# Kernel tuning notes

Hardware: AMD Instinct MI355X
Metric: run time of the kernel (lower is better)

The kernel has to match this reference:

```python
import jax, jax.numpy as jnp
import numpy as np

B, S, H, L, D, DI = 4, 32, 8, 128, 512, 2048
EPS = 1e-6
TEMP = float(D) ** 0.5


def layer_norm(x, g, b):
    mu = jnp.mean(x, axis=-1, keepdims=True)
    var = jnp.mean((x - mu) ** 2, axis=-1, keepdims=True)
    return (x - mu) * jax.lax.rsqrt(var + EPS) * g + b


def setup_inputs() -> dict:
    key = jax.random.key(0)
    ks = jax.random.split(key, 8)
    x = jax.random.normal(ks[0], (B, S, L, D), jnp.float32)
    mask = jax.random.randint(ks[1], (B, S, L), 0, 2, jnp.int32)
    # learned params
    w = jax.random.normal(ks[2], (1, 1, H, L, D), jnp.float32) * (1.0 / np.sqrt(D))
    v_w = jax.random.normal(ks[3], (D, D), jnp.float32) * 0.02   # nn.Linear weight (out,in)
    ln_g = jnp.ones((D,), jnp.float32)
    ln_b = jnp.zeros((D,), jnp.float32)
    w1 = jax.random.normal(ks[4], (DI, D), jnp.float32) * 0.02
    b1 = jnp.zeros((DI,), jnp.float32)
    w2 = jax.random.normal(ks[5], (D, DI), jnp.float32) * 0.02
    b2 = jnp.zeros((D,), jnp.float32)
    fln_g = jnp.ones((D,), jnp.float32)
    fln_b = jnp.zeros((D,), jnp.float32)
    return {"x": x, "mask": mask, "w": w, "v_w": v_w, "ln_g": ln_g, "ln_b": ln_b,
            "w1": w1, "b1": b1, "w2": w2, "b2": b2, "fln_g": fln_g, "fln_b": fln_b}


def reference(x, mask, w, v_w, ln_g, ln_b, w1, b1, w2, b2, fln_g, fln_b):
    # attn logits: broadcast mul + reduce over d_model == einsum over d
    attn = jnp.einsum('bsld,hld->bshl', x, w[0, 0]) / TEMP           # (B,S,H,L)
    attn = jnp.where(mask[:, :, None, :] == 0, -1e9, attn)
    attn = jax.nn.softmax(attn, axis=-1)                              # dropout: eval mode
    v = jnp.einsum('bsld,ed->bsle', x, v_w)                           # Linear no bias: x @ W.T
    out = jnp.einsum('bsld,bshl->bshd', v, attn)                      # weighted sum readout
    out = layer_norm(out, ln_g, ln_b)
    # PositionwiseFeedForward with residual + LayerNorm
    h = jax.nn.relu(jnp.einsum('bshd,fd->bshf', out, w1) + b1)
    y = jnp.einsum('bshf,df->bshd', h, w2) + b2 + out
    y = layer_norm(y, fln_g, fln_b)
    return y, attn
```

## Files before the change

### kernel.cpp

```cpp
#include <hip/hip_runtime.h>
#include <hip/hip_bf16.h>

#define BB 4
#define SS 32
#define HH 8
#define LL 128
#define DD 512
#define DI 2048
#define EPSN 1e-6f
#define INV_TEMP 0.04419417382415922f

#define NLOGIT_BLK 4096
#define NCAST_GRAN ((DI*DD/4)*2 + (DD*DD/4))
#define NCAST_BLK (NCAST_GRAN / 256)

#define NROW (BB*SS*HH)
#define SLICE ((size_t)NROW * DD)

typedef __attribute__((ext_vector_type(8))) short short8;
typedef __attribute__((ext_vector_type(4))) float float4v;

static __device__ __forceinline__ unsigned short f2b(float f) {
  __hip_bfloat16 h = __float2bfloat16(f);
  return *(unsigned short*)&h;
}

__global__ __launch_bounds__(256) void pre_kernel(
    const float* __restrict__ x, const int* __restrict__ mask,
    const float* __restrict__ w, const float* __restrict__ w1,
    const float* __restrict__ w2, const float* __restrict__ v_w,
    unsigned short* __restrict__ w1b, unsigned short* __restrict__ w2b,
    unsigned short* __restrict__ v_wb, float* __restrict__ logits) {
  int blk = blockIdx.x;
  if (blk < NLOGIT_BLK) {
    int wv = threadIdx.x >> 6, lane = threadIdx.x & 63;
    int p  = blk * 4 + wv;
    int bs = p >> 7, l = p & (LL - 1);

    const float4* xr = (const float4*)(x + ((size_t)bs * LL + l) * DD) + lane * 2;
    float4 x0 = xr[0], x1 = xr[1];

    float acc[HH];
#pragma unroll
    for (int h = 0; h < HH; ++h) {
      const float4* wr = (const float4*)(w + ((size_t)h * LL + l) * DD) + lane * 2;
      float4 w0 = wr[0], w1v = wr[1];
      acc[h] = x0.x * w0.x + x0.y * w0.y + x0.z * w0.z + x0.w * w0.w +
               x1.x * w1v.x + x1.y * w1v.y + x1.z * w1v.z + x1.w * w1v.w;
    }
#pragma unroll
    for (int off = 32; off > 0; off >>= 1) {
#pragma unroll
      for (int h = 0; h < HH; ++h) acc[h] += __shfl_xor(acc[h], off);
    }
    if (lane == 0) {
      int msk = mask[bs * LL + l];
#pragma unroll
      for (int h = 0; h < HH; ++h) {
        float lg = msk ? acc[h] * INV_TEMP : -1e9f;
        logits[((size_t)bs * HH + h) * LL + l] = lg;
      }
    }
  } else {
    const int n1 = (DI * DD) / 4;
    const int n2 = n1;
    int i = (blk - NLOGIT_BLK) * 256 + threadIdx.x;
    const float4* src;
    unsigned short* dst;
    int j = i;
    if (i < n1)           { src = (const float4*)w1;  dst = w1b; }
    else if (i < n1 + n2) { src = (const float4*)w2;  dst = w2b;  j = i - n1; }
    else                  { src = (const float4*)v_w; dst = v_wb; j = i - n1 - n2; }
    float4 v = src[j];
    dst[j * 4 + 0] = f2b(v.x);
    dst[j * 4 + 1] = f2b(v.y);
    dst[j * 4 + 2] = f2b(v.z);
    dst[j * 4 + 3] = f2b(v.w);
  }
}

__global__ __launch_bounds__(512) void xa_kernel(
    const float* __restrict__ x, const float* __restrict__ logits,
    float* __restrict__ attn_out, unsigned short* __restrict__ xab) {
  int bs = blockIdx.x >> 1, half = blockIdx.x & 1;
  int t = threadIdx.x, wv = t >> 6, lane = t & 63;

  __shared__ float sattn_t[LL][HH];
  __shared__ float sxa[2][HH][256];

  if (wv < 4) {
    for (int h = wv; h < HH; h += 4) {
      const float* lg = logits + ((size_t)bs * HH + h) * LL;
      float v0 = lg[lane], v1 = lg[lane + 64];
      float m = fmaxf(v0, v1);
#pragma unroll
      for (int off = 32; off > 0; off >>= 1) m = fmaxf(m, __shfl_xor(m, off));
      float e0 = __expf(v0 - m), e1 = __expf(v1 - m);
      float s = e0 + e1;
#pragma unroll
      for (int off = 32; off > 0; off >>= 1) s += __shfl_xor(s, off);
      float inv = 1.f / s;
      e0 *= inv; e1 *= inv;
      sattn_t[lane][h]      = e0;
      sattn_t[lane + 64][h] = e1;
      if (half == 0) {
        float* ao = attn_out + ((size_t)bs * HH + h) * LL;
        ao[lane]      = e0;
        ao[lane + 64] = e1;
      }
    }
  }
  __syncthreads();

  int col = t & 255, lseg = t >> 8;
  int e = half * 256 + col;
  const float* xb = x + (size_t)bs * LL * DD;
  float acc[HH];
#pragma unroll
  for (int h = 0; h < HH; ++h) acc[h] = 0.f;
  int l0 = lseg * 64;
  for (int l = l0; l < l0 + 64; ++l) {
    float xv = xb[(size_t)l * DD + e];
    float4 a0 = *(const float4*)&sattn_t[l][0];
    float4 a1 = *(const float4*)&sattn_t[l][4];
    acc[0] += a0.x * xv; acc[1] += a0.y * xv;
    acc[2] += a0.z * xv; acc[3] += a0.w * xv;
    acc[4] += a1.x * xv; acc[5] += a1.y * xv;
    acc[6] += a1.z * xv; acc[7] += a1.w * xv;
  }
#pragma unroll
  for (int h = 0; h < HH; ++h) sxa[lseg][h][col] = acc[h];
  __syncthreads();
  if (t < 256) {
    unsigned short* xo = xab + (size_t)bs * HH * DD;
#pragma unroll
    for (int h = 0; h < HH; ++h)
      xo[h * DD + t + half * 256] = f2b(sxa[0][h][t] + sxa[1][h][t]);
  }
}

__global__ __launch_bounds__(256) void gemm_v_kernel(
    const unsigned short* __restrict__ xab, const unsigned short* __restrict__ v_wb,
    float* __restrict__ vpart) {
  int blk = blockIdx.x;
  int nt = blk & 7, mt = (blk >> 3) & 15, kslice = blk >> 7;
  int wv = threadIdx.x >> 6, lane = threadIdx.x & 63;
  int lm = lane & 15, lq = lane >> 4;

  int m0 = mt * 64 + wv * 16;
  int n0 = nt * 64;
  int g0 = kslice * 16;

  const short8* A0 = (const short8*)(xab + (size_t)(m0 + lm) * DD) + g0;
  const short8* Bp[4];
#pragma unroll
  for (int nf = 0; nf < 4; ++nf)
    Bp[nf] = (const short8*)(v_wb + (size_t)(n0 + nf * 16 + lm) * DD) + g0;

  float4v acc[4];
#pragma unroll
  for (int nf = 0; nf < 4; ++nf) acc[nf] = (float4v){0.f, 0.f, 0.f, 0.f};

#pragma unroll
  for (int ks = 0; ks < 4; ++ks) {
    short8 a0 = A0[ks * 4 + lq];
    short8 b[4];
#pragma unroll
    for (int nf = 0; nf < 4; ++nf) b[nf] = Bp[nf][ks * 4 + lq];
#pragma unroll
    for (int nf = 0; nf < 4; ++nf)
      acc[nf] = __builtin_amdgcn_mfma_f32_16x16x32_bf16(a0, b[nf], acc[nf], 0, 0, 0);
  }

  float* outp = vpart + (size_t)kslice * SLICE;
#pragma unroll
  for (int nf = 0; nf < 4; ++nf) {
    int col = n0 + nf * 16 + lm;
#pragma unroll
    for (int r = 0; r < 4; ++r) {
      int row = m0 + lq * 4 + r;
      outp[(size_t)row * DD + col] = acc[nf][r];
    }
  }
}

__global__ __launch_bounds__(256) void ln_mid_kernel(
    const float* __restrict__ vpart, const float* __restrict__ ln_g,
    const float* __restrict__ ln_b, float* __restrict__ o_ln,
    unsigned short* __restrict__ o_lnb) {
  int wv = threadIdx.x >> 6, lane = threadIdx.x & 63;
  int row = blockIdx.x * 4 + wv;

  const float* p0 = vpart + (size_t)row * DD;
  float vals[8];
  float sum = 0.f, sq = 0.f;
#pragma unroll
  for (int k = 0; k < 8; ++k) {
    int d = lane + 64 * k;
    float v = p0[d] + p0[SLICE + d] + p0[2 * SLICE + d] + p0[3 * SLICE + d];
    vals[k] = v;
    sum += v;
    sq += v * v;
  }
#pragma unroll
  for (int off = 32; off > 0; off >>= 1) {
    sum += __shfl_xor(sum, off);
    sq  += __shfl_xor(sq, off);
  }
  float mu  = sum * (1.f / DD);
  float var = sq * (1.f / DD) - mu * mu;
  float rs  = rsqrtf(var + EPSN);
  float* op = o_ln + (size_t)row * DD;
  unsigned short* opb = o_lnb + (size_t)row * DD;
#pragma unroll
  for (int k = 0; k < 8; ++k) {
    int d = lane + 64 * k;
    float v = (vals[k] - mu) * rs * ln_g[d] + ln_b[d];
    op[d]  = v;
    opb[d] = f2b(v);
  }
}

__global__ __launch_bounds__(256) void gemm1_kernel(
    const unsigned short* __restrict__ xb, const unsigned short* __restrict__ w1b,
    const float* __restrict__ b1, unsigned short* __restrict__ h1b) {
  int blk = blockIdx.x;
  int nt = blk & 31, mt = blk >> 5;
  int wv = threadIdx.x >> 6, lane = threadIdx.x & 63;
  int lm = lane & 15, lq = lane >> 4;

  int m0 = mt * 64 + wv * 16;
  int n0 = nt * 64;

  const short8* A0 = (const short8*)(xb + (size_t)(m0 + lm) * DD);
  const short8* Bp[4];
#pragma unroll
  for (int nf = 0; nf < 4; ++nf)
    Bp[nf] = (const short8*)(w1b + (size_t)(n0 + nf * 16 + lm) * DD);

  float4v acc[4];
#pragma unroll
  for (int nf = 0; nf < 4; ++nf) acc[nf] = (float4v){0.f, 0.f, 0.f, 0.f};

#pragma unroll 4
  for (int ks = 0; ks < DD / 32; ++ks) {
    short8 a0 = A0[ks * 4 + lq];
    short8 b[4];
#pragma unroll
    for (int nf = 0; nf < 4; ++nf) b[nf] = Bp[nf][ks * 4 + lq];
#pragma unroll
    for (int nf = 0; nf < 4; ++nf)
      acc[nf] = __builtin_amdgcn_mfma_f32_16x16x32_bf16(a0, b[nf], acc[nf], 0, 0, 0);
  }

#pragma unroll
  for (int nf = 0; nf < 4; ++nf) {
    int col = n0 + nf * 16 + lm;
    float bb = b1[col];
#pragma unroll
    for (int r = 0; r < 4; ++r) {
      int row = m0 + lq * 4 + r;
      float v = acc[nf][r] + bb;
      h1b[(size_t)row * DI + col] = f2b(fmaxf(v, 0.f));
    }
  }
}

__global__ __launch_bounds__(256) void gemm2_kernel(
    const unsigned short* __restrict__ h1b, const unsigned short* __restrict__ w2b,
    float* __restrict__ ypart) {
  int blk = blockIdx.x;
  int nt = blk & 7, mt = (blk >> 3) & 15, kslice = blk >> 7;
  int wv = threadIdx.x >> 6, lane = threadIdx.x & 63;
  int lm = lane & 15, lq = lane >> 4;

  int m0 = mt * 64 + wv * 16;
  int n0 = nt * 64;
  int g0 = kslice * 64;

  const short8* A0 = (const short8*)(h1b + (size_t)(m0 + lm) * DI) + g0;
  const short8* Bp[4];
#pragma unroll
  for (int nf = 0; nf < 4; ++nf)
    Bp[nf] = (const short8*)(w2b + (size_t)(n0 + nf * 16 + lm) * DI) + g0;

  float4v acc[4];
#pragma unroll
  for (int nf = 0; nf < 4; ++nf) acc[nf] = (float4v){0.f, 0.f, 0.f, 0.f};

#pragma unroll 4
  for (int ks = 0; ks < 16; ++ks) {
    short8 a0 = A0[ks * 4 + lq];
    short8 b[4];
#pragma unroll
    for (int nf = 0; nf < 4; ++nf) b[nf] = Bp[nf][ks * 4 + lq];
#pragma unroll
    for (int nf = 0; nf < 4; ++nf)
      acc[nf] = __builtin_amdgcn_mfma_f32_16x16x32_bf16(a0, b[nf], acc[nf], 0, 0, 0);
  }

  float* outp = ypart + (size_t)kslice * SLICE;
#pragma unroll
  for (int nf = 0; nf < 4; ++nf) {
    int col = n0 + nf * 16 + lm;
#pragma unroll
    for (int r = 0; r < 4; ++r) {
      int row = m0 + lq * 4 + r;
      outp[(size_t)row * DD + col] = acc[nf][r];
    }
  }
}

__global__ __launch_bounds__(256) void ln_final_kernel(
    const float* __restrict__ ypart, const float* __restrict__ o_ln,
    const float* __restrict__ b2, const float* __restrict__ fln_g,
    const float* __restrict__ fln_b, float* __restrict__ y_out) {
  int wv = threadIdx.x >> 6, lane = threadIdx.x & 63;
  int row = blockIdx.x * 4 + wv;

  const float* p0 = ypart + (size_t)row * DD;
  const float* ol = o_ln + (size_t)row * DD;
  float vals[8];
  float sum = 0.f, sq = 0.f;
#pragma unroll
  for (int k = 0; k < 8; ++k) {
    int d = lane + 64 * k;
    float v = p0[d] + p0[SLICE + d] + p0[2 * SLICE + d] + p0[3 * SLICE + d] +
              b2[d] + ol[d];
    vals[k] = v;
    sum += v;
    sq += v * v;
  }
#pragma unroll
  for (int off = 32; off > 0; off >>= 1) {
    sum += __shfl_xor(sum, off);
    sq  += __shfl_xor(sq, off);
  }
  float mu  = sum * (1.f / DD);
  float var = sq * (1.f / DD) - mu * mu;
  float rs  = rsqrtf(var + EPSN);
  float* yo = y_out + (size_t)row * DD;
#pragma unroll
  for (int k = 0; k < 8; ++k) {
    int d = lane + 64 * k;
    yo[d] = (vals[k] - mu) * rs * fln_g[d] + fln_b[d];
  }
}

extern "C" void kernel_launch(void* const* d_in, const int* in_sizes, int n_in,
                              void* d_out, int out_size, void* d_ws, size_t ws_size,
                              hipStream_t stream) {
  const float* x     = (const float*)d_in[0];
  const int*   mask  = (const int*)d_in[1];
  const float* w     = (const float*)d_in[2];
  const float* v_w   = (const float*)d_in[3];
  const float* ln_g  = (const float*)d_in[4];
  const float* ln_b  = (const float*)d_in[5];
  const float* w1    = (const float*)d_in[6];
  const float* b1    = (const float*)d_in[7];
  const float* w2    = (const float*)d_in[8];
  const float* b2    = (const float*)d_in[9];
  const float* fln_g = (const float*)d_in[10];
  const float* fln_b = (const float*)d_in[11];

  float* y    = (float*)d_out;
  float* attn = y + (size_t)BB * SS * HH * DD;

  char* ws = (char*)d_ws;
  float*          o_ln    = (float*)(ws);
  unsigned short* o_lnb   = (unsigned short*)(ws + 2097152);
  unsigned short* w1b     = (unsigned short*)(ws + 3145728);
  unsigned short* w2b     = (unsigned short*)(ws + 5242880);
  unsigned short* h1b     = (unsigned short*)(ws + 7340032);
  float*          ypart   = (float*)(ws + 11534336);
  unsigned short* v_wb    = (unsigned short*)(ws + 19922944);
  unsigned short* xab     = (unsigned short*)(ws + 20447232);
  float*          vpart   = (float*)(ws + 21495808);
  float*          logits  = (float*)(ws + 29884416);

  pre_kernel<<<NLOGIT_BLK + NCAST_BLK, 256, 0, stream>>>(
      x, mask, w, w1, w2, v_w, w1b, w2b, v_wb, logits);
  xa_kernel<<<BB * SS * 2, 512, 0, stream>>>(x, logits, attn, xab);
  gemm_v_kernel<<<512, 256, 0, stream>>>(xab, v_wb, vpart);
  ln_mid_kernel<<<256, 256, 0, stream>>>(vpart, ln_g, ln_b, o_ln, o_lnb);
  gemm1_kernel<<<512, 256, 0, stream>>>(o_lnb, w1b, b1, h1b);
  gemm2_kernel<<<512, 256, 0, stream>>>(h1b, w2b, ypart);
  ln_final_kernel<<<256, 256, 0, stream>>>(ypart, o_ln, b2, fln_g, fln_b, y);
}
```

Before: 172.6 us.

## Fuse attention readout, V projection and mid LayerNorm into one kernel

Merges the softmax/attention-weighted x reduction, the bf16 MFMA V-projection GEMM and the first LayerNorm into a single kernel, one block per (b,s). The intermediate xa activations stay in shared memory as bf16 and the V output stays in shared memory in fp32, so the xab buffer, the split-K vpart partial sums and two kernel launches are no longer needed. The cost is less parallelism: 128 blocks instead of 256, each thread reducing over all 128 rows of x. Every block also re-reads the full V weight matrix through cache, and half of each MFMA A tile is padding rows whose results are thrown away.

```diff
diff --git a/kernel.cpp b/kernel.cpp
--- a/kernel.cpp
+++ b/kernel.cpp
@@ -16,6 +16,7 @@
 
 #define NROW (BB*SS*HH)
 #define SLICE ((size_t)NROW * DD)
+#define SXAP (DD + 8)
 
 typedef __attribute__((ext_vector_type(8))) short short8;
 typedef __attribute__((ext_vector_type(4))) float float4v;
@@ -79,14 +80,17 @@
   }
 }
 
-__global__ __launch_bounds__(512) void xa_kernel(
+__global__ __launch_bounds__(512) void xa_v_ln_kernel(
     const float* __restrict__ x, const float* __restrict__ logits,
-    float* __restrict__ attn_out, unsigned short* __restrict__ xab) {
-  int bs = blockIdx.x >> 1, half = blockIdx.x & 1;
+    const unsigned short* __restrict__ v_wb, const float* __restrict__ ln_g,
+    const float* __restrict__ ln_b, float* __restrict__ attn_out,
+    float* __restrict__ o_ln, unsigned short* __restrict__ o_lnb) {
+  int bs = blockIdx.x;
   int t = threadIdx.x, wv = t >> 6, lane = t & 63;
 
   __shared__ float sattn_t[LL][HH];
-  __shared__ float sxa[2][HH][256];
+  __shared__ unsigned short sxa[16][SXAP];
+  __shared__ float sout[HH][DD];
 
   if (wv < 4) {
     for (int h = wv; h < HH; h += 4) {
@@ -103,121 +107,96 @@
       e0 *= inv; e1 *= inv;
       sattn_t[lane][h]      = e0;
       sattn_t[lane + 64][h] = e1;
-      if (half == 0) {
-        float* ao = attn_out + ((size_t)bs * HH + h) * LL;
-        ao[lane]      = e0;
-        ao[lane + 64] = e1;
+      float* ao = attn_out + ((size_t)bs * HH + h) * LL;
+      ao[lane]      = e0;
+      ao[lane + 64] = e1;
+    }
+  }
+  __syncthreads();
+
+  {
+    int e = t;
+    const float* xb = x + (size_t)bs * LL * DD;
+    float acc[HH];
+#pragma unroll
+    for (int h = 0; h < HH; ++h) acc[h] = 0.f;
+    for (int l = 0; l < LL; ++l) {
+      float xv = xb[(size_t)l * DD + e];
+      float4 a0 = *(const float4*)&sattn_t[l][0];
+      float4 a1 = *(const float4*)&sattn_t[l][4];
+      acc[0] += a0.x * xv; acc[1] += a0.y * xv;
+      acc[2] += a0.z * xv; acc[3] += a0.w * xv;
+      acc[4] += a1.x * xv; acc[5] += a1.y * xv;
+      acc[6] += a1.z * xv; acc[7] += a1.w * xv;
+    }
+#pragma unroll
+    for (int h = 0; h < HH; ++h) sxa[h][e] = f2b(acc[h]);
+  }
+  __syncthreads();
+
+  {
+    int lm = lane & 15, lq = lane >> 4;
+    int n0 = wv * 64;
+    const short8* Bp[4];
+#pragma unroll
+    for (int nf = 0; nf < 4; ++nf)
+      Bp[nf] = (const short8*)(v_wb + (size_t)(n0 + nf * 16 + lm) * DD);
+
+    float4v acc[4];
+#pragma unroll
+    for (int nf = 0; nf < 4; ++nf) acc[nf] = (float4v){0.f, 0.f, 0.f, 0.f};
+
+#pragma unroll 4
+    for (int ks = 0; ks < DD / 32; ++ks) {
+      short8 a0 = *(const short8*)&sxa[lm][ks * 32 + lq * 8];
+      short8 b[4];
+#pragma unroll
+      for (int nf = 0; nf < 4; ++nf) b[nf] = Bp[nf][ks * 4 + lq];
+#pragma unroll
+      for (int nf = 0; nf < 4; ++nf)
+        acc[nf] = __builtin_amdgcn_mfma_f32_16x16x32_bf16(a0, b[nf], acc[nf], 0, 0, 0);
+    }
+
+#pragma unroll
+    for (int nf = 0; nf < 4; ++nf) {
+      int col = n0 + nf * 16 + lm;
+#pragma unroll
+      for (int r = 0; r < 4; ++r) {
+        int row = lq * 4 + r;
+        if (row < HH) sout[row][col] = acc[nf][r];
       }
     }
   }
   __syncthreads();
 
-  int col = t & 255, lseg = t >> 8;
-  int e = half * 256 + col;
-  const float* xb = x + (size_t)bs * LL * DD;
-  float acc[HH];
-#pragma unroll
-  for (int h = 0; h < HH; ++h) acc[h] = 0.f;
-  int l0 = lseg * 64;
-  for (int l = l0; l < l0 + 64; ++l) {
-    float xv = xb[(size_t)l * DD + e];
-    float4 a0 = *(const float4*)&sattn_t[l][0];
-    float4 a1 = *(const float4*)&sattn_t[l][4];
-    acc[0] += a0.x * xv; acc[1] += a0.y * xv;
-    acc[2] += a0.z * xv; acc[3] += a0.w * xv;
-    acc[4] += a1.x * xv; acc[5] += a1.y * xv;
-    acc[6] += a1.z * xv; acc[7] += a1.w * xv;
-  }
-#pragma unroll
-  for (int h = 0; h < HH; ++h) sxa[lseg][h][col] = acc[h];
-  __syncthreads();
-  if (t < 256) {
-    unsigned short* xo = xab + (size_t)bs * HH * DD;
-#pragma unroll
-    for (int h = 0; h < HH; ++h)
-      xo[h * DD + t + half * 256] = f2b(sxa[0][h][t] + sxa[1][h][t]);
-  }
-}
-
-__global__ __launch_bounds__(256) void gemm_v_kernel(
-    const unsigned short* __restrict__ xab, const unsigned short* __restrict__ v_wb,
-    float* __restrict__ vpart) {
-  int blk = blockIdx.x;
-  int nt = blk & 7, mt = (blk >> 3) & 15, kslice = blk >> 7;
-  int wv = threadIdx.x >> 6, lane = threadIdx.x & 63;
-  int lm = lane & 15, lq = lane >> 4;
-
-  int m0 = mt * 64 + wv * 16;
-  int n0 = nt * 64;
-  int g0 = kslice * 16;
-
-  const short8* A0 = (const short8*)(xab + (size_t)(m0 + lm) * DD) + g0;
-  const short8* Bp[4];
-#pragma unroll
-  for (int nf = 0; nf < 4; ++nf)
-    Bp[nf] = (const short8*)(v_wb + (size_t)(n0 + nf * 16 + lm) * DD) + g0;
-
-  float4v acc[4];
-#pragma unroll
-  for (int nf = 0; nf < 4; ++nf) acc[nf] = (float4v){0.f, 0.f, 0.f, 0.f};
-
-#pragma unroll
-  for (int ks = 0; ks < 4; ++ks) {
-    short8 a0 = A0[ks * 4 + lq];
-    short8 b[4];
-#pragma unroll
-    for (int nf = 0; nf < 4; ++nf) b[nf] = Bp[nf][ks * 4 + lq];
-#pragma unroll
-    for (int nf = 0; nf < 4; ++nf)
-      acc[nf] = __builtin_amdgcn_mfma_f32_16x16x32_bf16(a0, b[nf], acc[nf], 0, 0, 0);
-  }
-
-  float* outp = vpart + (size_t)kslice * SLICE;
-#pragma unroll
-  for (int nf = 0; nf < 4; ++nf) {
-    int col = n0 + nf * 16 + lm;
-#pragma unroll
-    for (int r = 0; r < 4; ++r) {
-      int row = m0 + lq * 4 + r;
-      outp[(size_t)row * DD + col] = acc[nf][r];
-    }
-  }
-}
-
-__global__ __launch_bounds__(256) void ln_mid_kernel(
-    const float* __restrict__ vpart, const float* __restrict__ ln_g,
-    const float* __restrict__ ln_b, float* __restrict__ o_ln,
-    unsigned short* __restrict__ o_lnb) {
-  int wv = threadIdx.x >> 6, lane = threadIdx.x & 63;
-  int row = blockIdx.x * 4 + wv;
-
-  const float* p0 = vpart + (size_t)row * DD;
-  float vals[8];
-  float sum = 0.f, sq = 0.f;
-#pragma unroll
-  for (int k = 0; k < 8; ++k) {
-    int d = lane + 64 * k;
-    float v = p0[d] + p0[SLICE + d] + p0[2 * SLICE + d] + p0[3 * SLICE + d];
-    vals[k] = v;
-    sum += v;
-    sq += v * v;
-  }
-#pragma unroll
-  for (int off = 32; off > 0; off >>= 1) {
-    sum += __shfl_xor(sum, off);
-    sq  += __shfl_xor(sq, off);
-  }
-  float mu  = sum * (1.f / DD);
-  float var = sq * (1.f / DD) - mu * mu;
-  float rs  = rsqrtf(var + EPSN);
-  float* op = o_ln + (size_t)row * DD;
-  unsigned short* opb = o_lnb + (size_t)row * DD;
-#pragma unroll
-  for (int k = 0; k < 8; ++k) {
-    int d = lane + 64 * k;
-    float v = (vals[k] - mu) * rs * ln_g[d] + ln_b[d];
-    op[d]  = v;
-    opb[d] = f2b(v);
+  {
+    int r = wv;
+    float vals[8];
+    float sum = 0.f, sq = 0.f;
+#pragma unroll
+    for (int k = 0; k < 8; ++k) {
+      float v = sout[r][lane + 64 * k];
+      vals[k] = v;
+      sum += v;
+      sq += v * v;
+    }
+#pragma unroll
+    for (int off = 32; off > 0; off >>= 1) {
+      sum += __shfl_xor(sum, off);
+      sq  += __shfl_xor(sq, off);
+    }
+    float mu  = sum * (1.f / DD);
+    float var = sq * (1.f / DD) - mu * mu;
+    float rs  = rsqrtf(var + EPSN);
+    float* op = o_ln + ((size_t)bs * HH + r) * DD;
+    unsigned short* opb = o_lnb + ((size_t)bs * HH + r) * DD;
+#pragma unroll
+    for (int k = 0; k < 8; ++k) {
+      int d = lane + 64 * k;
+      float v = (vals[k] - mu) * rs * ln_g[d] + ln_b[d];
+      op[d]  = v;
+      opb[d] = f2b(v);
+    }
   }
 }
 
@@ -374,15 +353,12 @@
   unsigned short* h1b     = (unsigned short*)(ws + 7340032);
   float*          ypart   = (float*)(ws + 11534336);
   unsigned short* v_wb    = (unsigned short*)(ws + 19922944);
-  unsigned short* xab     = (unsigned short*)(ws + 20447232);
-  float*          vpart   = (float*)(ws + 21495808);
-  float*          logits  = (float*)(ws + 29884416);
+  float*          logits  = (float*)(ws + 20447232);
 
   pre_kernel<<<NLOGIT_BLK + NCAST_BLK, 256, 0, stream>>>(
       x, mask, w, w1, w2, v_w, w1b, w2b, v_wb, logits);
-  xa_kernel<<<BB * SS * 2, 512, 0, stream>>>(x, logits, attn, xab);
-  gemm_v_kernel<<<512, 256, 0, stream>>>(xab, v_wb, vpart);
-  ln_mid_kernel<<<256, 256, 0, stream>>>(vpart, ln_g, ln_b, o_ln, o_lnb);
+  xa_v_ln_kernel<<<BB * SS, 512, 0, stream>>>(
+      x, logits, v_wb, ln_g, ln_b, attn, o_ln, o_lnb);
   gemm1_kernel<<<512, 256, 0, stream>>>(o_lnb, w1b, b1, h1b);
   gemm2_kernel<<<512, 256, 0, stream>>>(h1b, w2b, ypart);
   ln_final_kernel<<<256, 256, 0, stream>>>(ypart, o_ln, b2, fln_g, fln_b, y);
```

After: 181.0 us. 4.8% more time.

## Fuse seven kernel launches into one cooperative persistent megakernel with grid syncs

Applied to the files above, without the earlier changes.

Replaces the seven-kernel launch chain with a single cooperative kernel of 256 blocks by 512 threads. The stages (weight cast plus logits, softmax plus attention readout, V GEMM, mid LayerNorm, FFN GEMM1, GEMM2, final LayerNorm) are separated by grid.sync. The aim is to remove per-launch overhead and the gaps between kernels. In exchange each stage runs on a fixed 256-block grid with less parallelism and a different work split, for example 4x fewer waves for the logits stage. The LayerNorm stages leave most blocks idle, and grid syncs carry their own cost. The old multi-kernel path is kept as a fallback if cooperative launch is unavailable.

```diff
diff --git a/kernel.cpp b/kernel.cpp
--- a/kernel.cpp
+++ b/kernel.cpp
@@ -1,5 +1,8 @@
 #include <hip/hip_runtime.h>
 #include <hip/hip_bf16.h>
+#include <hip/hip_cooperative_groups.h>
+
+namespace cg = cooperative_groups;
 
 #define BB 4
 #define SS 32
@@ -10,12 +13,15 @@
 #define EPSN 1e-6f
 #define INV_TEMP 0.04419417382415922f
 
-#define NLOGIT_BLK 4096
 #define NCAST_GRAN ((DI*DD/4)*2 + (DD*DD/4))
-#define NCAST_BLK (NCAST_GRAN / 256)
-
 #define NROW (BB*SS*HH)
 #define SLICE ((size_t)NROW * DD)
+
+#define GRID 256
+#define BLK  512
+
+#define NLOGIT_BLK 4096
+#define NCAST_BLK (NCAST_GRAN / 256)
 
 typedef __attribute__((ext_vector_type(8))) short short8;
 typedef __attribute__((ext_vector_type(4))) float float4v;
@@ -23,6 +29,305 @@
 static __device__ __forceinline__ unsigned short f2b(float f) {
   __hip_bfloat16 h = __float2bfloat16(f);
   return *(unsigned short*)&h;
+}
+
+struct MegaParams {
+  const float* x; const int* mask; const float* w; const float* v_w;
+  const float* ln_g; const float* ln_b;
+  const float* w1; const float* b1; const float* w2; const float* b2;
+  const float* fln_g; const float* fln_b;
+  float* y; float* attn;
+  unsigned short* w1b; unsigned short* w2b; unsigned short* v_wb;
+  unsigned short* o_lnb; unsigned short* h1b; unsigned short* xab;
+  float* logits; float* o_ln; float* vpart; float* ypart;
+};
+
+__global__ __launch_bounds__(BLK, 2) void mega_kernel(MegaParams p) {
+  cg::grid_group grid = cg::this_grid();
+  int blk = blockIdx.x;
+  int t = threadIdx.x, wv = t >> 6, lane = t & 63;
+  int lm = lane & 15, lq = lane >> 4;
+
+  __shared__ float sattn_t[LL][HH];
+  __shared__ float sxa[2][HH][256];
+
+  {
+    const int n1 = (DI * DD) / 4;
+    const int n2 = n1;
+    for (int i = blk * BLK + t; i < NCAST_GRAN; i += GRID * BLK) {
+      const float4* src;
+      unsigned short* dst;
+      int j = i;
+      if (i < n1)           { src = (const float4*)p.w1;  dst = p.w1b; }
+      else if (i < n1 + n2) { src = (const float4*)p.w2;  dst = p.w2b;  j = i - n1; }
+      else                  { src = (const float4*)p.v_w; dst = p.v_wb; j = i - n1 - n2; }
+      float4 v = src[j];
+      dst[j * 4 + 0] = f2b(v.x);
+      dst[j * 4 + 1] = f2b(v.y);
+      dst[j * 4 + 2] = f2b(v.z);
+      dst[j * 4 + 3] = f2b(v.w);
+    }
+  }
+  {
+    int gw = blk * 8 + wv;
+#pragma unroll
+    for (int i = 0; i < 8; ++i) {
+      int pp = gw * 8 + i;
+      int bs = pp >> 7, l = pp & (LL - 1);
+      const float4* xr = (const float4*)(p.x + ((size_t)bs * LL + l) * DD) + lane * 2;
+      float4 x0 = xr[0], x1 = xr[1];
+      float acc[HH];
+#pragma unroll
+      for (int h = 0; h < HH; ++h) {
+        const float4* wr = (const float4*)(p.w + ((size_t)h * LL + l) * DD) + lane * 2;
+        float4 w0 = wr[0], w1v = wr[1];
+        acc[h] = x0.x * w0.x + x0.y * w0.y + x0.z * w0.z + x0.w * w0.w +
+                 x1.x * w1v.x + x1.y * w1v.y + x1.z * w1v.z + x1.w * w1v.w;
+      }
+#pragma unroll
+      for (int off = 32; off > 0; off >>= 1) {
+#pragma unroll
+        for (int h = 0; h < HH; ++h) acc[h] += __shfl_xor(acc[h], off);
+      }
+      if (lane == 0) {
+        int msk = p.mask[bs * LL + l];
+#pragma unroll
+        for (int h = 0; h < HH; ++h) {
+          float lg = msk ? acc[h] * INV_TEMP : -1e9f;
+          p.logits[((size_t)bs * HH + h) * LL + l] = lg;
+        }
+      }
+    }
+  }
+  grid.sync();
+
+  {
+    int bs = blk >> 1, half = blk & 1;
+    if (wv < 4) {
+      for (int h = wv; h < HH; h += 4) {
+        const float* lg = p.logits + ((size_t)bs * HH + h) * LL;
+        float v0 = lg[lane], v1 = lg[lane + 64];
+        float m = fmaxf(v0, v1);
+#pragma unroll
+        for (int off = 32; off > 0; off >>= 1) m = fmaxf(m, __shfl_xor(m, off));
+        float e0 = __expf(v0 - m), e1 = __expf(v1 - m);
+        float s = e0 + e1;
+#pragma unroll
+        for (int off = 32; off > 0; off >>= 1) s += __shfl_xor(s, off);
+        float inv = 1.f / s;
+        e0 *= inv; e1 *= inv;
+        sattn_t[lane][h]      = e0;
+        sattn_t[lane + 64][h] = e1;
+        if (half == 0) {
+          float* ao = p.attn + ((size_t)bs * HH + h) * LL;
+          ao[lane]      = e0;
+          ao[lane + 64] = e1;
+        }
+      }
+    }
+    __syncthreads();
+
+    int col = t & 255, lseg = t >> 8;
+    int e = half * 256 + col;
+    const float* xb = p.x + (size_t)bs * LL * DD;
+    float acc[HH];
+#pragma unroll
+    for (int h = 0; h < HH; ++h) acc[h] = 0.f;
+    int l0 = lseg * 64;
+    for (int l = l0; l < l0 + 64; ++l) {
+      float xv = xb[(size_t)l * DD + e];
+      float4 a0 = *(const float4*)&sattn_t[l][0];
+      float4 a1 = *(const float4*)&sattn_t[l][4];
+      acc[0] += a0.x * xv; acc[1] += a0.y * xv;
+      acc[2] += a0.z * xv; acc[3] += a0.w * xv;
+      acc[4] += a1.x * xv; acc[5] += a1.y * xv;
+      acc[6] += a1.z * xv; acc[7] += a1.w * xv;
+    }
+#pragma unroll
+    for (int h = 0; h < HH; ++h) sxa[lseg][h][col] = acc[h];
+    __syncthreads();
+    if (t < 256) {
+      unsigned short* xo = p.xab + (size_t)bs * HH * DD;
+#pragma unroll
+      for (int h = 0; h < HH; ++h)
+        xo[h * DD + t + half * 256] = f2b(sxa[0][h][t] + sxa[1][h][t]);
+    }
+  }
+  grid.sync();
+
+  {
+    int ks = blk >> 7, rem = blk & 127;
+    int mt = rem >> 3, nt = rem & 7;
+    int m0 = mt * 64 + (wv & 3) * 16;
+    int n0 = nt * 64 + (wv >> 2) * 32;
+    int g0 = ks * 32;
+
+    const short8* A0 = (const short8*)(p.xab + (size_t)(m0 + lm) * DD) + g0;
+    const short8* Bp[2];
+#pragma unroll
+    for (int nf = 0; nf < 2; ++nf)
+      Bp[nf] = (const short8*)(p.v_wb + (size_t)(n0 + nf * 16 + lm) * DD) + g0;
+
+    float4v acc[2];
+#pragma unroll
+    for (int nf = 0; nf < 2; ++nf) acc[nf] = (float4v){0.f, 0.f, 0.f, 0.f};
+#pragma unroll 4
+    for (int ksi = 0; ksi < 8; ++ksi) {
+      short8 a0 = A0[ksi * 4 + lq];
+      short8 b[2];
+#pragma unroll
+      for (int nf = 0; nf < 2; ++nf) b[nf] = Bp[nf][ksi * 4 + lq];
+#pragma unroll
+      for (int nf = 0; nf < 2; ++nf)
+        acc[nf] = __builtin_amdgcn_mfma_f32_16x16x32_bf16(a0, b[nf], acc[nf], 0, 0, 0);
+    }
+    float* outp = p.vpart + (size_t)ks * SLICE;
+#pragma unroll
+    for (int nf = 0; nf < 2; ++nf) {
+      int col = n0 + nf * 16 + lm;
+#pragma unroll
+      for (int r = 0; r < 4; ++r)
+        outp[(size_t)(m0 + lq * 4 + r) * DD + col] = acc[nf][r];
+    }
+  }
+  grid.sync();
+
+  if (blk < 128) {
+    int row = blk * 8 + wv;
+    const float* p0 = p.vpart + (size_t)row * DD;
+    float vals[8];
+    float sum = 0.f, sq = 0.f;
+#pragma unroll
+    for (int k = 0; k < 8; ++k) {
+      int d = lane + 64 * k;
+      float v = p0[d] + p0[SLICE + d];
+      vals[k] = v;
+      sum += v;
+      sq += v * v;
+    }
+#pragma unroll
+    for (int off = 32; off > 0; off >>= 1) {
+      sum += __shfl_xor(sum, off);
+      sq  += __shfl_xor(sq, off);
+    }
+    float mu  = sum * (1.f / DD);
+    float var = sq * (1.f / DD) - mu * mu;
+    float rs  = rsqrtf(var + EPSN);
+    float* op = p.o_ln + (size_t)row * DD;
+    unsigned short* opb = p.o_lnb + (size_t)row * DD;
+#pragma unroll
+    for (int k = 0; k < 8; ++k) {
+      int d = lane + 64 * k;
+      float v = (vals[k] - mu) * rs * p.ln_g[d] + p.ln_b[d];
+      op[d]  = v;
+      opb[d] = f2b(v);
+    }
+  }
+  grid.sync();
+
+  {
+    int mt = blk >> 4, nt = blk & 15;
+    int m0 = mt * 64 + (wv & 3) * 16;
+    int n0 = nt * 128 + (wv >> 2) * 64;
+
+    const short8* A0 = (const short8*)(p.o_lnb + (size_t)(m0 + lm) * DD);
+    const short8* Bp[4];
+#pragma unroll
+    for (int nf = 0; nf < 4; ++nf)
+      Bp[nf] = (const short8*)(p.w1b + (size_t)(n0 + nf * 16 + lm) * DD);
+
+    float4v acc[4];
+#pragma unroll
+    for (int nf = 0; nf < 4; ++nf) acc[nf] = (float4v){0.f, 0.f, 0.f, 0.f};
+#pragma unroll 4
+    for (int ksi = 0; ksi < DD / 32; ++ksi) {
+      short8 a0 = A0[ksi * 4 + lq];
+      short8 b[4];
+#pragma unroll
+      for (int nf = 0; nf < 4; ++nf) b[nf] = Bp[nf][ksi * 4 + lq];
+#pragma unroll
+      for (int nf = 0; nf < 4; ++nf)
+        acc[nf] = __builtin_amdgcn_mfma_f32_16x16x32_bf16(a0, b[nf], acc[nf], 0, 0, 0);
+    }
+#pragma unroll
+    for (int nf = 0; nf < 4; ++nf) {
+      int col = n0 + nf * 16 + lm;
+      float bb = p.b1[col];
+#pragma unroll
+      for (int r = 0; r < 4; ++r) {
+        float v = acc[nf][r] + bb;
+        p.h1b[(size_t)(m0 + lq * 4 + r) * DI + col] = f2b(fmaxf(v, 0.f));
+      }
+    }
+  }
+  grid.sync();
+
+  {
+    int ks = blk >> 7, rem = blk & 127;
+    int mt = rem >> 3, nt = rem & 7;
+    int m0 = mt * 64 + (wv & 3) * 16;
+    int n0 = nt * 64 + (wv >> 2) * 32;
+    int g0 = ks * 128;
+
+    const short8* A0 = (const short8*)(p.h1b + (size_t)(m0 + lm) * DI) + g0;
+    const short8* Bp[2];
+#pragma unroll
+    for (int nf = 0; nf < 2; ++nf)
+      Bp[nf] = (const short8*)(p.w2b + (size_t)(n0 + nf * 16 + lm) * DI) + g0;
+
+    float4v acc[2];
+#pragma unroll
+    for (int nf = 0; nf < 2; ++nf) acc[nf] = (float4v){0.f, 0.f, 0.f, 0.f};
+#pragma unroll 4
+    for (int ksi = 0; ksi < 32; ++ksi) {
+      short8 a0 = A0[ksi * 4 + lq];
+      short8 b[2];
+#pragma unroll
+      for (int nf = 0; nf < 2; ++nf) b[nf] = Bp[nf][ksi * 4 + lq];
+#pragma unroll
+      for (int nf = 0; nf < 2; ++nf)
+        acc[nf] = __builtin_amdgcn_mfma_f32_16x16x32_bf16(a0, b[nf], acc[nf], 0, 0, 0);
+    }
+    float* outp = p.ypart + (size_t)ks * SLICE;
+#pragma unroll
+    for (int nf = 0; nf < 2; ++nf) {
+      int col = n0 + nf * 16 + lm;
+#pragma unroll
+      for (int r = 0; r < 4; ++r)
+        outp[(size_t)(m0 + lq * 4 + r) * DD + col] = acc[nf][r];
+    }
+  }
+  grid.sync();
+
+  if (blk < 128) {
+    int row = blk * 8 + wv;
+    const float* p0 = p.ypart + (size_t)row * DD;
+    const float* ol = p.o_ln + (size_t)row * DD;
+    float vals[8];
+    float sum = 0.f, sq = 0.f;
+#pragma unroll
+    for (int k = 0; k < 8; ++k) {
+      int d = lane + 64 * k;
+      float v = p0[d] + p0[SLICE + d] + p.b2[d] + ol[d];
+      vals[k] = v;
+      sum += v;
+      sq += v * v;
+    }
+#pragma unroll
+    for (int off = 32; off > 0; off >>= 1) {
+      sum += __shfl_xor(sum, off);
+      sq  += __shfl_xor(sq, off);
+    }
+    float mu  = sum * (1.f / DD);
+    float var = sq * (1.f / DD) - mu * mu;
+    float rs  = rsqrtf(var + EPSN);
+    float* yo = p.y + (size_t)row * DD;
+#pragma unroll
+    for (int k = 0; k < 8; ++k) {
+      int d = lane + 64 * k;
+      yo[d] = (vals[k] - mu) * rs * p.fln_g[d] + p.fln_b[d];
+    }
+  }
 }
 
 __global__ __launch_bounds__(256) void pre_kernel(
@@ -350,40 +655,54 @@
 extern "C" void kernel_launch(void* const* d_in, const int* in_sizes, int n_in,
                               void* d_out, int out_size, void* d_ws, size_t ws_size,
                               hipStream_t stream) {
-  const float* x     = (const float*)d_in[0];
-  const int*   mask  = (const int*)d_in[1];
-  const float* w     = (const float*)d_in[2];
-  const float* v_w   = (const float*)d_in[3];
-  const float* ln_g  = (const float*)d_in[4];
-  const float* ln_b  = (const float*)d_in[5];
-  const float* w1    = (const float*)d_in[6];
-  const float* b1    = (const float*)d_in[7];
-  const float* w2    = (const float*)d_in[8];
-  const float* b2    = (const float*)d_in[9];
-  const float* fln_g = (const float*)d_in[10];
-  const float* fln_b = (const float*)d_in[11];
-
-  float* y    = (float*)d_out;
-  float* attn = y + (size_t)BB * SS * HH * DD;
+  MegaParams hp;
+  hp.x     = (const float*)d_in[0];
+  hp.mask  = (const int*)d_in[1];
+  hp.w     = (const float*)d_in[2];
+  hp.v_w   = (const float*)d_in[3];
+  hp.ln_g  = (const float*)d_in[4];
+  hp.ln_b  = (const float*)d_in[5];
+  hp.w1    = (const float*)d_in[6];
+  hp.b1    = (const float*)d_in[7];
+  hp.w2    = (const float*)d_in[8];
+  hp.b2    = (const float*)d_in[9];
+  hp.fln_g = (const float*)d_in[10];
+  hp.fln_b = (const float*)d_in[11];
+
+  hp.y    = (float*)d_out;
+  hp.attn = hp.y + (size_t)BB * SS * HH * DD;
 
   char* ws = (char*)d_ws;
-  float*          o_ln    = (float*)(ws);
-  unsigned short* o_lnb   = (unsigned short*)(ws + 2097152);
-  unsigned short* w1b     = (unsigned short*)(ws + 3145728);
-  unsigned short* w2b     = (unsigned short*)(ws + 5242880);
-  unsigned short* h1b     = (unsigned short*)(ws + 7340032);
-  float*          ypart   = (float*)(ws + 11534336);
-  unsigned short* v_wb    = (unsigned short*)(ws + 19922944);
-  unsigned short* xab     = (unsigned short*)(ws + 20447232);
-  float*          vpart   = (float*)(ws + 21495808);
-  float*          logits  = (float*)(ws + 29884416);
-
-  pre_kernel<<<NLOGIT_BLK + NCAST_BLK, 256, 0, stream>>>(
-      x, mask, w, w1, w2, v_w, w1b, w2b, v_wb, logits);
-  xa_kernel<<<BB * SS * 2, 512, 0, stream>>>(x, logits, attn, xab);
-  gemm_v_kernel<<<512, 256, 0, stream>>>(xab, v_wb, vpart);
-  ln_mid_kernel<<<256, 256, 0, stream>>>(vpart, ln_g, ln_b, o_ln, o_lnb);
-  gemm1_kernel<<<512, 256, 0, stream>>>(o_lnb, w1b, b1, h1b);
-  gemm2_kernel<<<512, 256, 0, stream>>>(h1b, w2b, ypart);
-  ln_final_kernel<<<256, 256, 0, stream>>>(ypart, o_ln, b2, fln_g, fln_b, y);
-}
+  hp.o_ln   = (float*)(ws);
+  hp.o_lnb  = (unsigned short*)(ws + 2097152);
+  hp.w1b    = (unsigned short*)(ws + 3145728);
+  hp.w2b    = (unsigned short*)(ws + 5242880);
+  hp.h1b    = (unsigned short*)(ws + 7340032);
+  hp.ypart  = (float*)(ws + 11534336);
+  hp.v_wb   = (unsigned short*)(ws + 19922944);
+  hp.xab    = (unsigned short*)(ws + 20447232);
+  hp.vpart  = (float*)(ws + 21495808);
+  hp.logits = (float*)(ws + 29884416);
+
+  hipError_t err = hipErrorUnknown;
+  int coop = 0;
+  if (hipDeviceGetAttribute(&coop, hipDeviceAttributeCooperativeLaunch, 0) ==
+          hipSuccess && coop) {
+    void* args[] = { &hp };
+    err = hipLaunchCooperativeKernel((const void*)mega_kernel, dim3(GRID),
+                                     dim3(BLK), args, 0, stream);
+  }
+  if (err != hipSuccess) {
+    pre_kernel<<<NLOGIT_BLK + NCAST_BLK, 256, 0, stream>>>(
+        hp.x, hp.mask, hp.w, hp.w1, hp.w2, hp.v_w, hp.w1b, hp.w2b, hp.v_wb,
+        hp.logits);
+    xa_kernel<<<BB * SS * 2, 512, 0, stream>>>(hp.x, hp.logits, hp.attn, hp.xab);
+    gemm_v_kernel<<<512, 256, 0, stream>>>(hp.xab, hp.v_wb, hp.vpart);
+    ln_mid_kernel<<<256, 256, 0, stream>>>(hp.vpart, hp.ln_g, hp.ln_b, hp.o_ln,
+                                           hp.o_lnb);
+    gemm1_kernel<<<512, 256, 0, stream>>>(hp.o_lnb, hp.w1b, hp.b1, hp.h1b);
+    gemm2_kernel<<<512, 256, 0, stream>>>(hp.h1b, hp.w2b, hp.ypart);
+    ln_final_kernel<<<256, 256, 0, stream>>>(hp.ypart, hp.o_ln, hp.b2,
+                                             hp.fln_g, hp.fln_b, hp.y);
+  }
+}
```

Measured after the change: 377.9 us. 119% more time.

## Fuse value GEMM, both LayerNorms and FFN into one per-sequence kernel

Applied to the files above, without the earlier changes.

Replaces the five kernels after attention (value projection, mid LayerNorm, FFN GEMM1, FFN GEMM2, final LayerNorm) with a single kernel. Each block owns one (b,s) pair's eight rows and keeps every intermediate in shared memory: the normalized activations, the 2048-wide hidden layer and the partial outputs. This removes four launches, the split-K partial buffers and their global round trips. The cost is that only 128 blocks run, each re-reading all bf16 weights from cache. Half of each 16-row MFMA tile is idle because there are only eight rows, and the residual now uses the bf16-rounded LayerNorm output.

```diff
diff --git a/kernel.cpp b/kernel.cpp
--- a/kernel.cpp
+++ b/kernel.cpp
@@ -14,8 +14,9 @@
 #define NCAST_GRAN ((DI*DD/4)*2 + (DD*DD/4))
 #define NCAST_BLK (NCAST_GRAN / 256)
 
-#define NROW (BB*SS*HH)
-#define SLICE ((size_t)NROW * DD)
+#define SAS 520
+#define H1S 2056
+#define SYS 516
 
 typedef __attribute__((ext_vector_type(8))) short short8;
 typedef __attribute__((ext_vector_type(4))) float float4v;
@@ -23,6 +24,11 @@
 static __device__ __forceinline__ unsigned short f2b(float f) {
   __hip_bfloat16 h = __float2bfloat16(f);
   return *(unsigned short*)&h;
+}
+static __device__ __forceinline__ float b2f(unsigned short u) {
+  union { unsigned int i; float f; } v;
+  v.i = ((unsigned int)u) << 16;
+  return v.f;
 }
 
 __global__ __launch_bounds__(256) void pre_kernel(
@@ -139,211 +145,145 @@
   }
 }
 
-__global__ __launch_bounds__(256) void gemm_v_kernel(
+__global__ __launch_bounds__(512, 4) void megaffn_kernel(
     const unsigned short* __restrict__ xab, const unsigned short* __restrict__ v_wb,
-    float* __restrict__ vpart) {
-  int blk = blockIdx.x;
-  int nt = blk & 7, mt = (blk >> 3) & 15, kslice = blk >> 7;
-  int wv = threadIdx.x >> 6, lane = threadIdx.x & 63;
+    const float* __restrict__ ln_g, const float* __restrict__ ln_b,
+    const unsigned short* __restrict__ w1b, const float* __restrict__ b1,
+    const unsigned short* __restrict__ w2b, const float* __restrict__ b2,
+    const float* __restrict__ fln_g, const float* __restrict__ fln_b,
+    float* __restrict__ y_out) {
+  int bs = blockIdx.x;
+  int t = threadIdx.x, wv = t >> 6, lane = t & 63;
   int lm = lane & 15, lq = lane >> 4;
 
-  int m0 = mt * 64 + wv * 16;
-  int n0 = nt * 64;
-  int g0 = kslice * 16;
-
-  const short8* A0 = (const short8*)(xab + (size_t)(m0 + lm) * DD) + g0;
-  const short8* Bp[4];
-#pragma unroll
-  for (int nf = 0; nf < 4; ++nf)
-    Bp[nf] = (const short8*)(v_wb + (size_t)(n0 + nf * 16 + lm) * DD) + g0;
-
-  float4v acc[4];
-#pragma unroll
-  for (int nf = 0; nf < 4; ++nf) acc[nf] = (float4v){0.f, 0.f, 0.f, 0.f};
-
-#pragma unroll
-  for (int ks = 0; ks < 4; ++ks) {
-    short8 a0 = A0[ks * 4 + lq];
-    short8 b[4];
-#pragma unroll
-    for (int nf = 0; nf < 4; ++nf) b[nf] = Bp[nf][ks * 4 + lq];
-#pragma unroll
-    for (int nf = 0; nf < 4; ++nf)
-      acc[nf] = __builtin_amdgcn_mfma_f32_16x16x32_bf16(a0, b[nf], acc[nf], 0, 0, 0);
-  }
-
-  float* outp = vpart + (size_t)kslice * SLICE;
-#pragma unroll
-  for (int nf = 0; nf < 4; ++nf) {
-    int col = n0 + nf * 16 + lm;
-#pragma unroll
-    for (int r = 0; r < 4; ++r) {
-      int row = m0 + lq * 4 + r;
-      outp[(size_t)row * DD + col] = acc[nf][r];
-    }
-  }
-}
-
-__global__ __launch_bounds__(256) void ln_mid_kernel(
-    const float* __restrict__ vpart, const float* __restrict__ ln_g,
-    const float* __restrict__ ln_b, float* __restrict__ o_ln,
-    unsigned short* __restrict__ o_lnb) {
-  int wv = threadIdx.x >> 6, lane = threadIdx.x & 63;
-  int row = blockIdx.x * 4 + wv;
-
-  const float* p0 = vpart + (size_t)row * DD;
-  float vals[8];
-  float sum = 0.f, sq = 0.f;
-#pragma unroll
-  for (int k = 0; k < 8; ++k) {
-    int d = lane + 64 * k;
-    float v = p0[d] + p0[SLICE + d] + p0[2 * SLICE + d] + p0[3 * SLICE + d];
-    vals[k] = v;
-    sum += v;
-    sq += v * v;
-  }
-#pragma unroll
-  for (int off = 32; off > 0; off >>= 1) {
-    sum += __shfl_xor(sum, off);
-    sq  += __shfl_xor(sq, off);
-  }
-  float mu  = sum * (1.f / DD);
-  float var = sq * (1.f / DD) - mu * mu;
-  float rs  = rsqrtf(var + EPSN);
-  float* op = o_ln + (size_t)row * DD;
-  unsigned short* opb = o_lnb + (size_t)row * DD;
-#pragma unroll
-  for (int k = 0; k < 8; ++k) {
-    int d = lane + 64 * k;
-    float v = (vals[k] - mu) * rs * ln_g[d] + ln_b[d];
-    op[d]  = v;
-    opb[d] = f2b(v);
-  }
-}
-
-__global__ __launch_bounds__(256) void gemm1_kernel(
-    const unsigned short* __restrict__ xb, const unsigned short* __restrict__ w1b,
-    const float* __restrict__ b1, unsigned short* __restrict__ h1b) {
-  int blk = blockIdx.x;
-  int nt = blk & 31, mt = blk >> 5;
-  int wv = threadIdx.x >> 6, lane = threadIdx.x & 63;
-  int lm = lane & 15, lq = lane >> 4;
-
-  int m0 = mt * 64 + wv * 16;
-  int n0 = nt * 64;
-
-  const short8* A0 = (const short8*)(xb + (size_t)(m0 + lm) * DD);
-  const short8* Bp[4];
-#pragma unroll
-  for (int nf = 0; nf < 4; ++nf)
-    Bp[nf] = (const short8*)(w1b + (size_t)(n0 + nf * 16 + lm) * DD);
-
-  float4v acc[4];
-#pragma unroll
-  for (int nf = 0; nf < 4; ++nf) acc[nf] = (float4v){0.f, 0.f, 0.f, 0.f};
-
-#pragma unroll 4
-  for (int ks = 0; ks < DD / 32; ++ks) {
-    short8 a0 = A0[ks * 4 + lq];
-    short8 b[4];
-#pragma unroll
-    for (int nf = 0; nf < 4; ++nf) b[nf] = Bp[nf][ks * 4 + lq];
-#pragma unroll
-    for (int nf = 0; nf < 4; ++nf)
-      acc[nf] = __builtin_amdgcn_mfma_f32_16x16x32_bf16(a0, b[nf], acc[nf], 0, 0, 0);
-  }
-
-#pragma unroll
-  for (int nf = 0; nf < 4; ++nf) {
-    int col = n0 + nf * 16 + lm;
-    float bb = b1[col];
-#pragma unroll
-    for (int r = 0; r < 4; ++r) {
-      int row = m0 + lq * 4 + r;
-      float v = acc[nf][r] + bb;
-      h1b[(size_t)row * DI + col] = f2b(fmaxf(v, 0.f));
-    }
-  }
-}
-
-__global__ __launch_bounds__(256) void gemm2_kernel(
-    const unsigned short* __restrict__ h1b, const unsigned short* __restrict__ w2b,
-    float* __restrict__ ypart) {
-  int blk = blockIdx.x;
-  int nt = blk & 7, mt = (blk >> 3) & 15, kslice = blk >> 7;
-  int wv = threadIdx.x >> 6, lane = threadIdx.x & 63;
-  int lm = lane & 15, lq = lane >> 4;
-
-  int m0 = mt * 64 + wv * 16;
-  int n0 = nt * 64;
-  int g0 = kslice * 64;
-
-  const short8* A0 = (const short8*)(h1b + (size_t)(m0 + lm) * DI) + g0;
-  const short8* Bp[4];
-#pragma unroll
-  for (int nf = 0; nf < 4; ++nf)
-    Bp[nf] = (const short8*)(w2b + (size_t)(n0 + nf * 16 + lm) * DI) + g0;
-
-  float4v acc[4];
-#pragma unroll
-  for (int nf = 0; nf < 4; ++nf) acc[nf] = (float4v){0.f, 0.f, 0.f, 0.f};
-
-#pragma unroll 4
-  for (int ks = 0; ks < 16; ++ks) {
-    short8 a0 = A0[ks * 4 + lq];
-    short8 b[4];
-#pragma unroll
-    for (int nf = 0; nf < 4; ++nf) b[nf] = Bp[nf][ks * 4 + lq];
-#pragma unroll
-    for (int nf = 0; nf < 4; ++nf)
-      acc[nf] = __builtin_amdgcn_mfma_f32_16x16x32_bf16(a0, b[nf], acc[nf], 0, 0, 0);
-  }
-
-  float* outp = ypart + (size_t)kslice * SLICE;
-#pragma unroll
-  for (int nf = 0; nf < 4; ++nf) {
-    int col = n0 + nf * 16 + lm;
-#pragma unroll
-    for (int r = 0; r < 4; ++r) {
-      int row = m0 + lq * 4 + r;
-      outp[(size_t)row * DD + col] = acc[nf][r];
-    }
-  }
-}
-
-__global__ __launch_bounds__(256) void ln_final_kernel(
-    const float* __restrict__ ypart, const float* __restrict__ o_ln,
-    const float* __restrict__ b2, const float* __restrict__ fln_g,
-    const float* __restrict__ fln_b, float* __restrict__ y_out) {
-  int wv = threadIdx.x >> 6, lane = threadIdx.x & 63;
-  int row = blockIdx.x * 4 + wv;
-
-  const float* p0 = ypart + (size_t)row * DD;
-  const float* ol = o_ln + (size_t)row * DD;
-  float vals[8];
-  float sum = 0.f, sq = 0.f;
-#pragma unroll
-  for (int k = 0; k < 8; ++k) {
-    int d = lane + 64 * k;
-    float v = p0[d] + p0[SLICE + d] + p0[2 * SLICE + d] + p0[3 * SLICE + d] +
-              b2[d] + ol[d];
-    vals[k] = v;
-    sum += v;
-    sq += v * v;
-  }
-#pragma unroll
-  for (int off = 32; off > 0; off >>= 1) {
-    sum += __shfl_xor(sum, off);
-    sq  += __shfl_xor(sq, off);
-  }
-  float mu  = sum * (1.f / DD);
-  float var = sq * (1.f / DD) - mu * mu;
-  float rs  = rsqrtf(var + EPSN);
-  float* yo = y_out + (size_t)row * DD;
-#pragma unroll
-  for (int k = 0; k < 8; ++k) {
-    int d = lane + 64 * k;
-    yo[d] = (vals[k] - mu) * rs * fln_g[d] + fln_b[d];
+  __shared__ __attribute__((aligned(16))) unsigned short sA[8 * SAS];
+  __shared__ __attribute__((aligned(16))) unsigned short h1[8 * H1S];
+  __shared__ __attribute__((aligned(16))) float sY[8 * SYS];
+
+  {
+    const short8* src = (const short8*)(xab + (size_t)bs * HH * DD);
+    short8 v = src[t];
+    *(short8*)&sA[(t >> 6) * SAS + (t & 63) * 8] = v;
+  }
+  __syncthreads();
+
+  int arow = (lm & 7) * SAS;
+
+  {
+    int n0 = wv * 64;
+#pragma unroll
+    for (int nf = 0; nf < 4; ++nf) {
+      int n = n0 + nf * 16 + lm;
+      const short8* B = (const short8*)(v_wb + (size_t)n * DD);
+      float4v acc = (float4v){0.f, 0.f, 0.f, 0.f};
+#pragma unroll
+      for (int ks = 0; ks < 16; ++ks) {
+        short8 a = *(const short8*)&sA[arow + ks * 32 + lq * 8];
+        acc = __builtin_amdgcn_mfma_f32_16x16x32_bf16(a, B[ks * 4 + lq], acc, 0, 0, 0);
+      }
+      if (lq < 2) {
+#pragma unroll
+        for (int r = 0; r < 4; ++r) sY[(lq * 4 + r) * SYS + n] = acc[r];
+      }
+    }
+  }
+  __syncthreads();
+
+  {
+    int row = wv;
+    float vals[8];
+    float sum = 0.f, sq = 0.f;
+#pragma unroll
+    for (int k = 0; k < 8; ++k) {
+      float v = sY[row * SYS + lane + 64 * k];
+      vals[k] = v;
+      sum += v;
+      sq += v * v;
+    }
+#pragma unroll
+    for (int off = 32; off > 0; off >>= 1) {
+      sum += __shfl_xor(sum, off);
+      sq  += __shfl_xor(sq, off);
+    }
+    float mu  = sum * (1.f / DD);
+    float var = sq * (1.f / DD) - mu * mu;
+    float rs  = rsqrtf(var + EPSN);
+#pragma unroll
+    for (int k = 0; k < 8; ++k) {
+      int d = lane + 64 * k;
+      sA[row * SAS + d] = f2b((vals[k] - mu) * rs * ln_g[d] + ln_b[d]);
+    }
+  }
+  __syncthreads();
+
+  {
+    int n0 = wv * 256;
+    for (int nf = 0; nf < 16; ++nf) {
+      int n = n0 + nf * 16 + lm;
+      const short8* B = (const short8*)(w1b + (size_t)n * DD);
+      float4v acc = (float4v){0.f, 0.f, 0.f, 0.f};
+#pragma unroll
+      for (int ks = 0; ks < 16; ++ks) {
+        short8 a = *(const short8*)&sA[arow + ks * 32 + lq * 8];
+        acc = __builtin_amdgcn_mfma_f32_16x16x32_bf16(a, B[ks * 4 + lq], acc, 0, 0, 0);
+      }
+      if (lq < 2) {
+        float bb = b1[n];
+#pragma unroll
+        for (int r = 0; r < 4; ++r)
+          h1[(lq * 4 + r) * H1S + n] = f2b(fmaxf(acc[r] + bb, 0.f));
+      }
+    }
+  }
+  __syncthreads();
+
+  {
+    int hrow = (lm & 7) * H1S;
+    int n0 = wv * 64;
+#pragma unroll
+    for (int nf = 0; nf < 4; ++nf) {
+      int n = n0 + nf * 16 + lm;
+      const short8* B = (const short8*)(w2b + (size_t)n * DI);
+      float4v acc = (float4v){0.f, 0.f, 0.f, 0.f};
+#pragma unroll 8
+      for (int ks = 0; ks < 64; ++ks) {
+        short8 a = *(const short8*)&h1[hrow + ks * 32 + lq * 8];
+        acc = __builtin_amdgcn_mfma_f32_16x16x32_bf16(a, B[ks * 4 + lq], acc, 0, 0, 0);
+      }
+      if (lq < 2) {
+#pragma unroll
+        for (int r = 0; r < 4; ++r) sY[(lq * 4 + r) * SYS + n] = acc[r];
+      }
+    }
+  }
+  __syncthreads();
+
+  {
+    int row = wv;
+    float vals[8];
+    float sum = 0.f, sq = 0.f;
+#pragma unroll
+    for (int k = 0; k < 8; ++k) {
+      int d = lane + 64 * k;
+      float v = sY[row * SYS + d] + b2[d] + b2f(sA[row * SAS + d]);
+      vals[k] = v;
+      sum += v;
+      sq += v * v;
+    }
+#pragma unroll
+    for (int off = 32; off > 0; off >>= 1) {
+      sum += __shfl_xor(sum, off);
+      sq  += __shfl_xor(sq, off);
+    }
+    float mu  = sum * (1.f / DD);
+    float var = sq * (1.f / DD) - mu * mu;
+    float rs  = rsqrtf(var + EPSN);
+    float* yo = y_out + ((size_t)bs * HH + row) * DD;
+#pragma unroll
+    for (int k = 0; k < 8; ++k) {
+      int d = lane + 64 * k;
+      yo[d] = (vals[k] - mu) * rs * fln_g[d] + fln_b[d];
+    }
   }
 }
 
@@ -367,23 +307,15 @@
   float* attn = y + (size_t)BB * SS * HH * DD;
 
   char* ws = (char*)d_ws;
-  float*          o_ln    = (float*)(ws);
-  unsigned short* o_lnb   = (unsigned short*)(ws + 2097152);
-  unsigned short* w1b     = (unsigned short*)(ws + 3145728);
-  unsigned short* w2b     = (unsigned short*)(ws + 5242880);
-  unsigned short* h1b     = (unsigned short*)(ws + 7340032);
-  float*          ypart   = (float*)(ws + 11534336);
-  unsigned short* v_wb    = (unsigned short*)(ws + 19922944);
-  unsigned short* xab     = (unsigned short*)(ws + 20447232);
-  float*          vpart   = (float*)(ws + 21495808);
-  float*          logits  = (float*)(ws + 29884416);
+  unsigned short* w1b    = (unsigned short*)(ws);
+  unsigned short* w2b    = (unsigned short*)(ws + 2097152);
+  unsigned short* v_wb   = (unsigned short*)(ws + 4194304);
+  unsigned short* xab    = (unsigned short*)(ws + 4718592);
+  float*          logits = (float*)(ws + 5767168);
 
   pre_kernel<<<NLOGIT_BLK + NCAST_BLK, 256, 0, stream>>>(
       x, mask, w, w1, w2, v_w, w1b, w2b, v_wb, logits);
   xa_kernel<<<BB * SS * 2, 512, 0, stream>>>(x, logits, attn, xab);
-  gemm_v_kernel<<<512, 256, 0, stream>>>(xab, v_wb, vpart);
-  ln_mid_kernel<<<256, 256, 0, stream>>>(vpart, ln_g, ln_b, o_ln, o_lnb);
-  gemm1_kernel<<<512, 256, 0, stream>>>(o_lnb, w1b, b1, h1b);
-  gemm2_kernel<<<512, 256, 0, stream>>>(h1b, w2b, ypart);
-  ln_final_kernel<<<256, 256, 0, stream>>>(ypart, o_ln, b2, fln_g, fln_b, y);
-}
+  megaffn_kernel<<<BB * SS, 512, 0, stream>>>(
+      xab, v_wb, ln_g, ln_b, w1b, b1, w2b, b2, fln_g, fln_b, y);
+}
```

Result: slower. 247.7 us (+43.5%).
